# Kernel optimization log

Measured on AMD Instinct MI355X. Metric: run time of the kernel, lower is better.

The kernel has to match this reference:

```python
import jax, jax.numpy as jnp
import numpy as np

DECAY = 0.8
CODEBOOK_SIZE = 1024
DIM = 128


def setup_inputs() -> dict:
    key = jax.random.key(0)
    k1, k2 = jax.random.split(key)
    x = jax.random.normal(k1, (16, 4096, DIM), dtype=jnp.float32)
    embed = jax.random.normal(k2, (CODEBOOK_SIZE, DIM), dtype=jnp.float32)
    ema_embed = embed * 1.0  # ema_num_initial = 1.0
    ema_num = jnp.ones((CODEBOOK_SIZE,), dtype=jnp.float32)
    return {"x": x, "embed": embed, "ema_embed": ema_embed, "ema_num": ema_num}


def reference(x, embed, ema_embed, ema_num):
    # flatten: [..., d] -> [N, d]
    shape = x.shape
    flatten = x.reshape(-1, shape[-1])  # [N, d]
    distance = -2.0 * (flatten @ embed.T) + jnp.sum(embed * embed, axis=-1)  # [N, K]
    embed_ind = jnp.argmin(distance, axis=-1)  # [N]
    quantize = embed[embed_ind.reshape(shape[:-1])]  # gather -> [..., d]

    # training branch: onehot^T @ flatten == segment_sum over code indices
    num_curr = jax.ops.segment_sum(
        jnp.ones_like(embed_ind, dtype=jnp.float32), embed_ind,
        num_segments=CODEBOOK_SIZE)  # [K]
    embed_curr = jax.ops.segment_sum(
        flatten.astype(jnp.float32), embed_ind,
        num_segments=CODEBOOK_SIZE)  # [K, d]

    ema_num_new = ema_num * DECAY + (1.0 - DECAY) * num_curr
    ema_embed_new = ema_embed * DECAY + (1.0 - DECAY) * embed_curr
    embed_new = ema_embed_new / ema_num_new[:, None]
    return quantize, embed_new, ema_embed_new, ema_num_new
```

## Files before the change

### kernel.cpp

```cpp
#include <hip/hip_runtime.h>

#define NPTS   65536
#define DIM    128
#define KCODES 1024
#define BM     128
#define TILE_C 64
#define NTHR   512

typedef short bf16x8 __attribute__((ext_vector_type(8)));
typedef float f32x4  __attribute__((ext_vector_type(4)));

__device__ __forceinline__ short f2bf(float f) {
    unsigned u = __builtin_bit_cast(unsigned, f);
    u = (u + 0x7fffu + ((u >> 16) & 1u)) >> 16;
    return (short)u;
}
__device__ __forceinline__ float bf2f(short s) {
    unsigned u = ((unsigned)(unsigned short)s) << 16;
    return __builtin_bit_cast(float, u);
}
__device__ __forceinline__ void gload_lds16(const void* g, void* l) {
    __builtin_amdgcn_global_load_lds(
        (const __attribute__((address_space(1))) void*)g,
        (__attribute__((address_space(3))) void*)l, 16, 0, 0);
}

__global__ __launch_bounds__(256)
void halfnorm_kernel(const float* __restrict__ embed, float* __restrict__ hn)
{
    const int w    = (blockIdx.x * blockDim.x + threadIdx.x) >> 6;
    const int lane = threadIdx.x & 63;
    if (w < KCODES) {
        float v0 = embed[(long)w * DIM + lane];
        float v1 = embed[(long)w * DIM + 64 + lane];
        float s  = v0 * v0 + v1 * v1;
        #pragma unroll
        for (int off = 32; off > 0; off >>= 1) s += __shfl_xor(s, off);
        if (lane == 0) hn[w] = 0.5f * s;
    }
}

__global__ __launch_bounds__(256)
void pack_kernel(const float* __restrict__ embed, short* __restrict__ ebf,
                 int* __restrict__ ghist, const float* __restrict__ ema_embed,
                 float* __restrict__ acc)
{
    const int g   = blockIdx.x * 256 + threadIdx.x;
    if (g < KCODES) ghist[g] = 0;
    {
        float4 e = reinterpret_cast<const float4*>(ema_embed)[g];
        float4 o = {0.8f * e.x, 0.8f * e.y, 0.8f * e.z, 0.8f * e.w};
        reinterpret_cast<float4*>(acc)[g] = o;
    }
    const int tc  = g >> 11;
    const int f   = (g >> 6) & 31;
    const int l   = g & 63;
    const int h   = f >> 4;
    const int nt  = (f >> 2) & 3;
    const int akk = f & 3;
    const int hg  = l >> 4;
    const int n   = l & 15;
    const int c   = tc * TILE_C + nt * 16 + n;
    const int d0  = akk * 32 + hg * 8;
    const float* src = embed + (long)c * DIM + d0;
    float4 v0 = *reinterpret_cast<const float4*>(src);
    float4 v1 = *reinterpret_cast<const float4*>(src + 4);
    float vv[8] = {v0.x, v0.y, v0.z, v0.w, v1.x, v1.y, v1.z, v1.w};
    bf16x8 out;
    #pragma unroll
    for (int j = 0; j < 8; ++j) {
        short hi = f2bf(vv[j]);
        out[j] = h ? f2bf(vv[j] - bf2f(hi)) : hi;
    }
    *reinterpret_cast<bf16x8*>(ebf + (long)g * 8) = out;
}

__global__ __launch_bounds__(NTHR, 2)
void argmin_kernel(const float* __restrict__ x, const short* __restrict__ ebf,
                   const float* __restrict__ halfnorm, const float* __restrict__ embed,
                   int* __restrict__ ind, float* __restrict__ quant,
                   int* __restrict__ ghist)
{
    __shared__ short es[2][16384];
    __shared__ float hn_lds[KCODES];
    __shared__ int   hist[KCODES];
    __shared__ int   bidx[BM];

    const int t    = threadIdx.x;
    const int lane = t & 63;
    const int w    = t >> 6;
    const int r16  = lane & 15;
    const int h4   = lane >> 4;
    const long xbase = (long)blockIdx.x * BM * DIM;
    const int  wp    = w * 16;

    for (int i = t; i < KCODES; i += NTHR) hist[i] = 0;

    bf16x8 ahi[4], alo[4];
    {
        const long prow = xbase + (long)(wp + r16) * DIM;
        #pragma unroll
        for (int kk = 0; kk < 4; ++kk) {
            const float* s = x + prow + kk * 32 + h4 * 8;
            float4 u0 = *reinterpret_cast<const float4*>(s);
            float4 u1 = *reinterpret_cast<const float4*>(s + 4);
            float vv[8] = {u0.x, u0.y, u0.z, u0.w, u1.x, u1.y, u1.z, u1.w};
            #pragma unroll
            for (int j = 0; j < 8; ++j) {
                short hi = f2bf(vv[j]);
                ahi[kk][j] = hi;
                alo[kk][j] = f2bf(vv[j] - bf2f(hi));
            }
        }
    }
    if (t < 256) reinterpret_cast<float4*>(hn_lds)[t] =
                 reinterpret_cast<const float4*>(halfnorm)[t];

    #pragma unroll
    for (int i = 0; i < 4; ++i) {
        const int f = w * 4 + i;
        gload_lds16(ebf + (long)f * 512 + lane * 8, &es[0][f * 512]);
    }
    __syncthreads();

    float bestv[4];
    int   besti[4];
    #pragma unroll
    for (int s = 0; s < 4; ++s) { bestv[s] = -1e30f; besti[s] = 0; }

    for (int tile = 0; tile < KCODES / TILE_C; ++tile) {
        if (tile + 1 < KCODES / TILE_C) {
            const long gbase = (long)(tile + 1) * 16384;
            #pragma unroll
            for (int i = 0; i < 4; ++i) {
                const int f = w * 4 + i;
                gload_lds16(ebf + gbase + f * 512 + lane * 8, &es[(tile + 1) & 1][f * 512]);
            }
        }

        const short* buf = es[tile & 1];
        f32x4 C[4];
        #pragma unroll
        for (int nt = 0; nt < 4; ++nt) C[nt] = (f32x4){0.f, 0.f, 0.f, 0.f};

        #pragma unroll
        for (int akk = 0; akk < 4; ++akk) {
            #pragma unroll
            for (int nt = 0; nt < 4; ++nt) {
                bf16x8 Bh = *reinterpret_cast<const bf16x8*>(buf + (nt * 4 + akk) * 512 + lane * 8);
                C[nt] = __builtin_amdgcn_mfma_f32_16x16x32_bf16(ahi[akk], Bh, C[nt], 0, 0, 0);
                C[nt] = __builtin_amdgcn_mfma_f32_16x16x32_bf16(alo[akk], Bh, C[nt], 0, 0, 0);
                bf16x8 Bl = *reinterpret_cast<const bf16x8*>(buf + (16 + nt * 4 + akk) * 512 + lane * 8);
                C[nt] = __builtin_amdgcn_mfma_f32_16x16x32_bf16(ahi[akk], Bl, C[nt], 0, 0, 0);
            }
        }

        #pragma unroll
        for (int nt = 0; nt < 4; ++nt) {
            const int   c   = tile * TILE_C + nt * 16 + r16;
            const float hnv = hn_lds[c];
            #pragma unroll
            for (int reg = 0; reg < 4; ++reg) {
                float sc = C[nt][reg] - hnv;
                if (sc > bestv[reg]) { bestv[reg] = sc; besti[reg] = c; }
            }
        }
        __syncthreads();
    }

    #pragma unroll
    for (int s = 0; s < 4; ++s) {
        float v = bestv[s];
        int   i = besti[s];
        #pragma unroll
        for (int off = 1; off < 16; off <<= 1) {
            float ov = __shfl_xor(v, off);
            int   oi = __shfl_xor(i, off);
            if (ov > v || (ov == v && oi < i)) { v = ov; i = oi; }
        }
        bestv[s] = v; besti[s] = i;
    }
    if (r16 == 0) {
        #pragma unroll
        for (int s = 0; s < 4; ++s) {
            int p = wp + h4 * 4 + s;
            bidx[p] = besti[s];
            ind[blockIdx.x * BM + p] = besti[s];
        }
    }
    __syncthreads();

    if (t < BM) atomicAdd(&hist[bidx[t]], 1);

    float4* dst = reinterpret_cast<float4*>(quant + xbase);
    #pragma unroll
    for (int i = 0; i < 8; ++i) {
        int idx = i * NTHR + t;
        int p   = idx >> 5;
        int q   = idx & 31;
        int c   = bidx[p];
        dst[idx] = reinterpret_cast<const float4*>(embed + (long)c * DIM)[q];
    }

    __syncthreads();
    for (int i = t; i < KCODES; i += NTHR)
        if (hist[i]) atomicAdd(&ghist[i], hist[i]);
}

__global__ __launch_bounds__(1024)
void scan_kernel(const int* __restrict__ ghist, const float* __restrict__ ema_num,
                 float* __restrict__ ema_num_new, int* __restrict__ cursor)
{
    __shared__ int tmp[KCODES];
    const int t = threadIdx.x;
    const int v = ghist[t];
    ema_num_new[t] = ema_num[t] * 0.8f + 0.2f * (float)v;
    tmp[t] = v;
    __syncthreads();
    #pragma unroll
    for (int off = 1; off < KCODES; off <<= 1) {
        int u = (t >= off) ? tmp[t - off] : 0;
        __syncthreads();
        tmp[t] += u;
        __syncthreads();
    }
    cursor[t] = tmp[t] - v;
}

__global__ __launch_bounds__(256)
void scatter_kernel(const int* __restrict__ ind, int* __restrict__ cursor,
                    int* __restrict__ sorted, int* __restrict__ scode)
{
    const int p = blockIdx.x * 256 + threadIdx.x;
    const int c = ind[p];
    const int pos = atomicAdd(&cursor[c], 1);
    sorted[pos] = p;
    scode[pos]  = c;
}

__global__ __launch_bounds__(128)
void sum2_kernel(const float* __restrict__ x, const int* __restrict__ sorted,
                 const int* __restrict__ scode, float* __restrict__ acc)
{
    __shared__ int sp[64];
    __shared__ int sc[64];
    const int t = threadIdx.x;
    const int base = blockIdx.x * 64;
    if (t < 64) { sp[t] = sorted[base + t]; sc[t] = scode[base + t]; }
    __syncthreads();

    float a = 0.f;
    int cprev = sc[0];
    #pragma unroll 1
    for (int kk = 0; kk < 8; ++kk) {
        float v[8];
        #pragma unroll
        for (int i = 0; i < 8; ++i)
            v[i] = x[(long)sp[kk * 8 + i] * DIM + t];
        #pragma unroll
        for (int i = 0; i < 8; ++i) {
            const int c = sc[kk * 8 + i];
            if (c != cprev) {
                atomicAdd(&acc[(long)cprev * DIM + t], 0.2f * a);
                a = 0.f; cprev = c;
            }
            a += v[i];
        }
    }
    atomicAdd(&acc[(long)cprev * DIM + t], 0.2f * a);
}

__global__ __launch_bounds__(256)
void final_kernel(const float* __restrict__ acc, const float* __restrict__ ema_num_new,
                  float* __restrict__ embed_new)
{
    const int g = blockIdx.x * 256 + threadIdx.x;
    float4 v = reinterpret_cast<const float4*>(acc)[g];
    const float en = ema_num_new[g >> 5];
    float4 o = {v.x / en, v.y / en, v.z / en, v.w / en};
    reinterpret_cast<float4*>(embed_new)[g] = o;
}

extern "C" void kernel_launch(void* const* d_in, const int* in_sizes, int n_in,
                              void* d_out, int out_size, void* d_ws, size_t ws_size,
                              hipStream_t stream)
{
    const float* x         = (const float*)d_in[0];
    const float* embed     = (const float*)d_in[1];
    const float* ema_embed = (const float*)d_in[2];
    const float* ema_num   = (const float*)d_in[3];

    float* out0 = (float*)d_out;
    float* out1 = out0 + 8388608;
    float* out2 = out1 + 131072;
    float* out3 = out2 + 131072;

    char*  ws     = (char*)d_ws;
    float* hn     = (float*)ws;
    int*   ind    = (int*)(ws + 4096);
    short* ebf    = (short*)(ws + 266240);
    int*   ghist  = (int*)(ws + 790528);
    int*   cursor = (int*)(ws + 794624);
    int*   sorted = (int*)(ws + 798720);
    int*   scode  = (int*)(ws + 1060864);

    halfnorm_kernel<<<256, 256, 0, stream>>>(embed, hn);
    pack_kernel<<<128, 256, 0, stream>>>(embed, ebf, ghist, ema_embed, out2);
    argmin_kernel<<<NPTS / BM, NTHR, 0, stream>>>(x, ebf, hn, embed, ind, out0, ghist);
    scan_kernel<<<1, 1024, 0, stream>>>(ghist, ema_num, out3, cursor);
    scatter_kernel<<<NPTS / 256, 256, 0, stream>>>(ind, cursor, sorted, scode);
    sum2_kernel<<<NPTS / 64, 128, 0, stream>>>(x, sorted, scode, out2);
    final_kernel<<<128, 256, 0, stream>>>(out2, out3, out1);
}
```

Baseline: 112.2 us.

## Halve block threads and have each wave compute two 16-row M subtiles

```diff
diff --git a/kernel.cpp b/kernel.cpp
--- a/kernel.cpp
+++ b/kernel.cpp
@@ -5,7 +5,7 @@
 #define KCODES 1024
 #define BM     128
 #define TILE_C 64
-#define NTHR   512
+#define NTHR   256
 
 typedef short bf16x8 __attribute__((ext_vector_type(8)));
 typedef float f32x4  __attribute__((ext_vector_type(4)));
@@ -92,13 +92,14 @@
     const int r16  = lane & 15;
     const int h4   = lane >> 4;
     const long xbase = (long)blockIdx.x * BM * DIM;
-    const int  wp    = w * 16;
+    const int  wp    = w * 32;
 
     for (int i = t; i < KCODES; i += NTHR) hist[i] = 0;
 
-    bf16x8 ahi[4], alo[4];
-    {
-        const long prow = xbase + (long)(wp + r16) * DIM;
+    bf16x8 ahi[2][4], alo[2][4];
+    #pragma unroll
+    for (int ms = 0; ms < 2; ++ms) {
+        const long prow = xbase + (long)(wp + ms * 16 + r16) * DIM;
         #pragma unroll
         for (int kk = 0; kk < 4; ++kk) {
             const float* s = x + prow + kk * 32 + h4 * 8;
@@ -108,50 +109,54 @@
             #pragma unroll
             for (int j = 0; j < 8; ++j) {
                 short hi = f2bf(vv[j]);
-                ahi[kk][j] = hi;
-                alo[kk][j] = f2bf(vv[j] - bf2f(hi));
+                ahi[ms][kk][j] = hi;
+                alo[ms][kk][j] = f2bf(vv[j] - bf2f(hi));
             }
         }
     }
-    if (t < 256) reinterpret_cast<float4*>(hn_lds)[t] =
-                 reinterpret_cast<const float4*>(halfnorm)[t];
-
-    #pragma unroll
-    for (int i = 0; i < 4; ++i) {
-        const int f = w * 4 + i;
+    reinterpret_cast<float4*>(hn_lds)[t] = reinterpret_cast<const float4*>(halfnorm)[t];
+
+    #pragma unroll
+    for (int i = 0; i < 8; ++i) {
+        const int f = w * 8 + i;
         gload_lds16(ebf + (long)f * 512 + lane * 8, &es[0][f * 512]);
     }
     __syncthreads();
 
-    float bestv[4];
-    int   besti[4];
-    #pragma unroll
-    for (int s = 0; s < 4; ++s) { bestv[s] = -1e30f; besti[s] = 0; }
+    float bestv[8];
+    int   besti[8];
+    #pragma unroll
+    for (int s = 0; s < 8; ++s) { bestv[s] = -1e30f; besti[s] = 0; }
 
     for (int tile = 0; tile < KCODES / TILE_C; ++tile) {
         if (tile + 1 < KCODES / TILE_C) {
             const long gbase = (long)(tile + 1) * 16384;
             #pragma unroll
-            for (int i = 0; i < 4; ++i) {
-                const int f = w * 4 + i;
+            for (int i = 0; i < 8; ++i) {
+                const int f = w * 8 + i;
                 gload_lds16(ebf + gbase + f * 512 + lane * 8, &es[(tile + 1) & 1][f * 512]);
             }
         }
 
         const short* buf = es[tile & 1];
-        f32x4 C[4];
-        #pragma unroll
-        for (int nt = 0; nt < 4; ++nt) C[nt] = (f32x4){0.f, 0.f, 0.f, 0.f};
+        f32x4 C[4][2];
+        #pragma unroll
+        for (int nt = 0; nt < 4; ++nt)
+            #pragma unroll
+            for (int ms = 0; ms < 2; ++ms) C[nt][ms] = (f32x4){0.f, 0.f, 0.f, 0.f};
 
         #pragma unroll
         for (int akk = 0; akk < 4; ++akk) {
             #pragma unroll
             for (int nt = 0; nt < 4; ++nt) {
                 bf16x8 Bh = *reinterpret_cast<const bf16x8*>(buf + (nt * 4 + akk) * 512 + lane * 8);
-                C[nt] = __builtin_amdgcn_mfma_f32_16x16x32_bf16(ahi[akk], Bh, C[nt], 0, 0, 0);
-                C[nt] = __builtin_amdgcn_mfma_f32_16x16x32_bf16(alo[akk], Bh, C[nt], 0, 0, 0);
                 bf16x8 Bl = *reinterpret_cast<const bf16x8*>(buf + (16 + nt * 4 + akk) * 512 + lane * 8);
-                C[nt] = __builtin_amdgcn_mfma_f32_16x16x32_bf16(ahi[akk], Bl, C[nt], 0, 0, 0);
+                C[nt][0] = __builtin_amdgcn_mfma_f32_16x16x32_bf16(ahi[0][akk], Bh, C[nt][0], 0, 0, 0);
+                C[nt][1] = __builtin_amdgcn_mfma_f32_16x16x32_bf16(ahi[1][akk], Bh, C[nt][1], 0, 0, 0);
+                C[nt][0] = __builtin_amdgcn_mfma_f32_16x16x32_bf16(alo[0][akk], Bh, C[nt][0], 0, 0, 0);
+                C[nt][1] = __builtin_amdgcn_mfma_f32_16x16x32_bf16(alo[1][akk], Bh, C[nt][1], 0, 0, 0);
+                C[nt][0] = __builtin_amdgcn_mfma_f32_16x16x32_bf16(ahi[0][akk], Bl, C[nt][0], 0, 0, 0);
+                C[nt][1] = __builtin_amdgcn_mfma_f32_16x16x32_bf16(ahi[1][akk], Bl, C[nt][1], 0, 0, 0);
             }
         }
 
@@ -160,16 +165,19 @@
             const int   c   = tile * TILE_C + nt * 16 + r16;
             const float hnv = hn_lds[c];
             #pragma unroll
-            for (int reg = 0; reg < 4; ++reg) {
-                float sc = C[nt][reg] - hnv;
-                if (sc > bestv[reg]) { bestv[reg] = sc; besti[reg] = c; }
-            }
+            for (int ms = 0; ms < 2; ++ms)
+                #pragma unroll
+                for (int reg = 0; reg < 4; ++reg) {
+                    float sc  = C[nt][ms][reg] - hnv;
+                    int  slot = ms * 4 + reg;
+                    if (sc > bestv[slot]) { bestv[slot] = sc; besti[slot] = c; }
+                }
         }
         __syncthreads();
     }
 
     #pragma unroll
-    for (int s = 0; s < 4; ++s) {
+    for (int s = 0; s < 8; ++s) {
         float v = bestv[s];
         int   i = besti[s];
         #pragma unroll
@@ -182,8 +190,9 @@
     }
     if (r16 == 0) {
         #pragma unroll
-        for (int s = 0; s < 4; ++s) {
-            int p = wp + h4 * 4 + s;
+        for (int s = 0; s < 8; ++s) {
+            int ms = s >> 2, reg = s & 3;
+            int p  = wp + ms * 16 + h4 * 4 + reg;
             bidx[p] = besti[s];
             ind[blockIdx.x * BM + p] = besti[s];
         }
@@ -194,7 +203,7 @@
 
     float4* dst = reinterpret_cast<float4*>(quant + xbase);
     #pragma unroll
-    for (int i = 0; i < 8; ++i) {
+    for (int i = 0; i < 16; ++i) {
         int idx = i * NTHR + t;
         int p   = idx >> 5;
         int q   = idx & 31;
```

Measured after the change: 112.9 us. No clear change (+0.6%).
